# Kernel optimization log

Hardware: AMD Instinct MI355X
Metric: run time of the kernel (lower is better)

## Reference

```python
import jax, jax.numpy as jnp
import numpy as np

HEADS = 16
DIM_HEAD = 64
EPS = 1e-12  # F.normalize default eps


def setup_inputs() -> dict:
    key = jax.random.key(0)
    k1, k2, k3 = jax.random.split(key, 3)
    b, n, dim = 2, 2048, 1024
    dim_inner = HEADS * DIM_HEAD
    x = jax.random.normal(k1, (b, n, dim), dtype=jnp.float32)
    gamma = jnp.ones((dim,), dtype=jnp.float32)
    w_qkv = jax.random.normal(k2, (dim, 3 * dim_inner), dtype=jnp.float32) * 0.02
    w_out = jax.random.normal(k3, (dim_inner, dim), dtype=jnp.float32) * 0.02
    return {"x": x, "gamma": gamma, "w_qkv": w_qkv, "w_out": w_out}


def reference(x, gamma, w_qkv, w_out):
    b, n, dim = x.shape
    h, d = HEADS, DIM_HEAD
    scale = d ** -0.5

    # RMSNorm (lucidrains): F.normalize(x, dim=-1) * dim**0.5 * gamma
    norm = jnp.sqrt(jnp.sum(x * x, axis=-1, keepdims=True))
    xn = x / jnp.maximum(norm, EPS) * (dim ** 0.5) * gamma

    # qkv projection -> [b, n, 3, h, d] -> q/k/v each [b, h, n, d]
    qkv = (xn @ w_qkv).reshape(b, n, 3, h, d)
    qkv = jnp.transpose(qkv, (2, 0, 3, 1, 4))
    q, k, v = qkv[0], qkv[1], qkv[2]

    q = q * scale
    sim = jnp.einsum('bhid,bhjd->bhij', q, k)  # [b, h, n, n]
    causal_mask = jnp.triu(jnp.ones((n, n), dtype=bool), k=1)
    mask_value = -jnp.finfo(sim.dtype).max
    sim = jnp.where(causal_mask, mask_value, sim)
    attn = jax.nn.softmax(sim, axis=-1)
    out = jnp.einsum('bhij,bhjd->bhid', attn, v)  # [b, h, n, d]

    out = jnp.transpose(out, (0, 2, 1, 3)).reshape(b, n, h * d)
    return out @ w_out
```

## Files before the change

kernel.cpp:

```cpp
#include <hip/hip_runtime.h>

typedef __attribute__((ext_vector_type(8))) short bf16x8;
typedef __attribute__((ext_vector_type(4))) short bf16x4;
typedef __attribute__((ext_vector_type(4))) float f32x4;

static __device__ __forceinline__ short f2bf(float f) {
    union { float f; unsigned u; } v; v.f = f;
    unsigned r = v.u + 0x7fffu + ((v.u >> 16) & 1u);
    return (short)(r >> 16);
}

static __device__ __forceinline__ void async_copy16(const short* g, short* l) {
    __builtin_amdgcn_global_load_lds((const __attribute__((address_space(1))) void*)g,
                                     (__attribute__((address_space(3))) void*)l,
                                     16, 0, 0);
}

#define HEADS 16
#define DHEAD 64
#define NSEQ  2048
#define DIM   1024
#define BATCH 2
#define ROWS  (BATCH * NSEQ)
#define NQKV  (3 * HEADS * DHEAD)

__global__ __launch_bounds__(256) void prep_kernel(const float* __restrict__ x,
                                                   const float* __restrict__ gamma,
                                                   const float* __restrict__ w_qkv,
                                                   const float* __restrict__ w_out,
                                                   short* __restrict__ xn,
                                                   short* __restrict__ wqkvT,
                                                   short* __restrict__ woutT) {
    const int blk = blockIdx.x;
    const int t = threadIdx.x;
    __shared__ float tile[64][65];
    __shared__ float part[4];

    if (blk < 1024) {
        const float* in;  short* out;  int C, bx, by;
        if (blk < 768) { in = w_qkv; out = wqkvT; C = NQKV; bx = blk % 48; by = blk / 48; }
        else           { in = w_out; out = woutT; C = DIM;  bx = (blk - 768) & 15; by = (blk - 768) >> 4; }
        const int gx = bx * 64, gy = by * 64;
        const int lc4 = (t & 15) * 4;
        const int lr  = t >> 4;
#pragma unroll
        for (int p = 0; p < 4; ++p) {
            const float4 v = *(const float4*)&in[(size_t)(gy + p * 16 + lr) * C + gx + lc4];
            tile[p * 16 + lr][lc4 + 0] = v.x;
            tile[p * 16 + lr][lc4 + 1] = v.y;
            tile[p * 16 + lr][lc4 + 2] = v.z;
            tile[p * 16 + lr][lc4 + 3] = v.w;
        }
        __syncthreads();
        const int oc  = t >> 2;
        const int or4 = (t & 3) * 16;
#pragma unroll
        for (int j = 0; j < 4; ++j) {
            bf16x4 w;
#pragma unroll
            for (int r = 0; r < 4; ++r) w[r] = f2bf(tile[or4 + j * 4 + r][oc]);
            *(bf16x4*)&out[(size_t)(gx + oc) * DIM + gy + or4 + j * 4] = w;
        }
    } else {
        const int row = blk - 1024;
        const float4 v = ((const float4*)(x + (size_t)row * DIM))[t];
        float s = v.x * v.x + v.y * v.y + v.z * v.z + v.w * v.w;
#pragma unroll
        for (int off = 32; off > 0; off >>= 1) s += __shfl_down(s, off, 64);
        if ((t & 63) == 0) part[t >> 6] = s;
        __syncthreads();
        const float tot = part[0] + part[1] + part[2] + part[3];
        const float scale = 32.0f / fmaxf(sqrtf(tot), 1e-12f);
        const float4 g = ((const float4*)gamma)[t];
        bf16x4 o;
        o[0] = f2bf(v.x * scale * g.x);
        o[1] = f2bf(v.y * scale * g.y);
        o[2] = f2bf(v.z * scale * g.z);
        o[3] = f2bf(v.w * scale * g.w);
        *(bf16x4*)(xn + (size_t)row * DIM + t * 4) = o;
    }
}

template <int MODE, int MT, int NT, int WM, int WN>
__global__ __launch_bounds__(256) void gemm_bt(const short* __restrict__ A,
                                               const short* __restrict__ Bt,
                                               void* __restrict__ Cout,
                                               short* __restrict__ vtOut,
                                               int K, int N) {
    constexpr int TM = WM * MT * 16;
    constexpr int TN = WN * NT * 16;
    __shared__ alignas(16) short lds_a[2][TM * 32];
    __shared__ alignas(16) short lds_b[2][TN * 32];
    const int tid = threadIdx.x;
    const int lane = tid & 63, wid = tid >> 6;
    const int quad = lane >> 4, l16 = lane & 15;
    const int wm = wid / WN, wn = wid % WN;

    const int nx = gridDim.x;
    const int nwg = nx * gridDim.y;
    int flat = blockIdx.y * nx + blockIdx.x;
    if ((nwg & 7) == 0) {
        const int q8 = nwg >> 3;
        flat = (flat & 7) * q8 + (flat >> 3);
    }
    const int mb = (flat / nx) * TM, nb = (flat % nx) * TN;

    f32x4 acc[MT][NT];
#pragma unroll
    for (int i = 0; i < MT; ++i)
#pragma unroll
        for (int j = 0; j < NT; ++j) acc[i][j] = (f32x4){0.f, 0.f, 0.f, 0.f};

    const int lr = lane >> 2;
    const int lc = (lane & 3) * 8;

    auto stage = [&](int kb, int buf) {
#pragma unroll
        for (int c = 0; c < TM / 64; ++c) {
            const int row = c * 64 + wid * 16 + lr;
            async_copy16(&A[(size_t)(mb + row) * K + kb + lc], &lds_a[buf][row * 32 + lc]);
        }
#pragma unroll
        for (int c = 0; c < TN / 64; ++c) {
            const int row = c * 64 + wid * 16 + lr;
            async_copy16(&Bt[(size_t)(nb + row) * K + kb + lc], &lds_b[buf][row * 32 + lc]);
        }
    };

    stage(0, 0);
    __syncthreads();

    int cur = 0;
    for (int kb = 0; kb < K; kb += 32) {
        if (kb + 32 < K) stage(kb + 32, cur ^ 1);

        bf16x8 af[MT], bfr[NT];
#pragma unroll
        for (int mt = 0; mt < MT; ++mt)
            af[mt] = *(const bf16x8*)&lds_a[cur][(wm * MT * 16 + mt * 16 + l16) * 32 + quad * 8];
#pragma unroll
        for (int nt = 0; nt < NT; ++nt)
            bfr[nt] = *(const bf16x8*)&lds_b[cur][(wn * NT * 16 + nt * 16 + l16) * 32 + quad * 8];
#pragma unroll
        for (int mt = 0; mt < MT; ++mt)
#pragma unroll
            for (int nt = 0; nt < NT; ++nt)
                acc[mt][nt] = __builtin_amdgcn_mfma_f32_16x16x32_bf16(af[mt], bfr[nt],
                                                                      acc[mt][nt], 0, 0, 0);

        __syncthreads();
        cur ^= 1;
    }

#pragma unroll
    for (int mt = 0; mt < MT; ++mt) {
#pragma unroll
        for (int nt = 0; nt < NT; ++nt) {
            const int grow0 = mb + wm * MT * 16 + mt * 16 + quad * 4;
            const int gcol  = nb + wn * NT * 16 + nt * 16 + l16;
            if (MODE == 0) {
                const int s3 = gcol >> 10, rem = gcol & 1023;
                const int hh = rem >> 6, dd = rem & 63;
                const int bb = grow0 >> 11, npos0 = grow0 & 2047;
                if (s3 == 2) {
                    bf16x4 vw;
#pragma unroll
                    for (int r = 0; r < 4; ++r) vw[r] = f2bf(acc[mt][nt][r]);
                    *(bf16x4*)&vtOut[((size_t)(bb * 16 + hh) * 64 + dd) * 2048 + npos0] = vw;
                } else {
                    const float sc = (s3 == 0) ? 0.125f : 1.0f;
#pragma unroll
                    for (int r = 0; r < 4; ++r)
                        ((short*)Cout)[(size_t)((s3 * 32 + bb * 16 + hh) * 2048 + npos0 + r) * 64 +
                                       dd] = f2bf(acc[mt][nt][r] * sc);
                }
            } else {
#pragma unroll
                for (int r = 0; r < 4; ++r)
                    ((float*)Cout)[(size_t)(grow0 + r) * N + gcol] = acc[mt][nt][r];
            }
        }
    }
}

__global__ __launch_bounds__(256, 3) void attn_kernel(const short* __restrict__ qg,
                                                      const short* __restrict__ kg,
                                                      const short* __restrict__ vtg,
                                                      short* __restrict__ og) {
    const int tid = threadIdx.x;
    const int wid = tid >> 6, lane = tid & 63;
    const int quad = lane >> 4, l16 = lane & 15;
    const int blk = blockIdx.x;
    const int qt = 15 - (blk >> 5);
    const int bh = blk & 31;
    const size_t base = (size_t)bh * (NSEQ * DHEAD);
    const int bb = bh >> 4, hh = bh & 15;
    const int qbase = qt * 128 + wid * 32;
    const int ntiles = 2 * qt + 2;

    __shared__ alignas(16) short kA[2][2048], kB[2][2048];
    __shared__ alignas(16) short vA[2][2048], vB[2][2048];
    __shared__ alignas(16) short pbuf[4][32 * 72];
    short* const pb = pbuf[wid];

    const int sr = tid >> 2;
    const int sc = (tid & 3) * 8;
    auto stage = [&](int t, short (&KB_)[2][2048], short (&VB_)[2][2048]) {
        const int kb = t * 64;
        async_copy16(&kg[base + (size_t)(kb + sr) * 64 + sc],      &KB_[0][sr * 32 + sc]);
        async_copy16(&kg[base + (size_t)(kb + sr) * 64 + 32 + sc], &KB_[1][sr * 32 + sc]);
        async_copy16(&vtg[base + (size_t)sr * 2048 + kb + sc],      &VB_[0][sr * 32 + sc]);
        async_copy16(&vtg[base + (size_t)sr * 2048 + kb + 32 + sc], &VB_[1][sr * 32 + sc]);
    };

    bf16x8 qf[2][2];
#pragma unroll
    for (int qn = 0; qn < 2; ++qn)
#pragma unroll
        for (int kh = 0; kh < 2; ++kh)
            qf[qn][kh] = *(const bf16x8*)&qg[base + (size_t)(qbase + qn * 16 + l16) * DHEAD +
                                            kh * 32 + quad * 8];

    float li[2] = {0.f, 0.f};
    f32x4 accO[2][4];
#pragma unroll
    for (int qn = 0; qn < 2; ++qn)
#pragma unroll
        for (int nc = 0; nc < 4; ++nc) accO[qn][nc] = (f32x4){0.f, 0.f, 0.f, 0.f};

    auto tile_step = [&](const short (&KB_)[2][2048], const short (&VB_)[2][2048], int t) {
        const int kb = t * 64;
        f32x4 sf[2][4];
#pragma unroll
        for (int m = 0; m < 4; ++m) {
            const bf16x8 kf0 = *(const bf16x8*)&KB_[0][(m * 16 + l16) * 32 + quad * 8];
            const bf16x8 kf1 = *(const bf16x8*)&KB_[1][(m * 16 + l16) * 32 + quad * 8];
#pragma unroll
            for (int qn = 0; qn < 2; ++qn) {
                f32x4 z = (f32x4){0.f, 0.f, 0.f, 0.f};
                z = __builtin_amdgcn_mfma_f32_16x16x32_bf16(kf0, qf[qn][0], z, 0, 0, 0);
                sf[qn][m] = __builtin_amdgcn_mfma_f32_16x16x32_bf16(kf1, qf[qn][1], z, 0, 0, 0);
            }
        }
        if (kb + 64 > qbase) {
#pragma unroll
            for (int qn = 0; qn < 2; ++qn) {
                const int myq = qbase + qn * 16 + l16;
#pragma unroll
                for (int m = 0; m < 4; ++m)
#pragma unroll
                    for (int r = 0; r < 4; ++r)
                        if (kb + m * 16 + quad * 4 + r > myq) sf[qn][m][r] = -3.0e38f;
            }
        }
#pragma unroll
        for (int qn = 0; qn < 2; ++qn) {
            float rs = 0.f;
#pragma unroll
            for (int m = 0; m < 4; ++m) {
                bf16x4 pw;
#pragma unroll
                for (int r = 0; r < 4; ++r) {
                    const float p = __expf(sf[qn][m][r]);
                    rs += p;
                    pw[r] = f2bf(p);
                }
                *(bf16x4*)&pb[(qn * 16 + l16) * 72 + m * 16 + quad * 4] = pw;
            }
            li[qn] += rs;
        }
        bf16x8 pf[2][2];
#pragma unroll
        for (int qn = 0; qn < 2; ++qn)
#pragma unroll
            for (int ks = 0; ks < 2; ++ks)
                pf[qn][ks] = *(const bf16x8*)&pb[(qn * 16 + l16) * 72 + ks * 32 + quad * 8];
#pragma unroll
        for (int nc = 0; nc < 4; ++nc) {
            const bf16x8 vf0 = *(const bf16x8*)&VB_[0][(nc * 16 + l16) * 32 + quad * 8];
            const bf16x8 vf1 = *(const bf16x8*)&VB_[1][(nc * 16 + l16) * 32 + quad * 8];
#pragma unroll
            for (int qn = 0; qn < 2; ++qn) {
                accO[qn][nc] = __builtin_amdgcn_mfma_f32_16x16x32_bf16(vf0, pf[qn][0],
                                                                      accO[qn][nc], 0, 0, 0);
                accO[qn][nc] = __builtin_amdgcn_mfma_f32_16x16x32_bf16(vf1, pf[qn][1],
                                                                      accO[qn][nc], 0, 0, 0);
            }
        }
    };

    stage(0, kA, vA);
    __syncthreads();
    for (int t = 0; t < ntiles; t += 2) {
        stage(t + 1, kB, vB);
        tile_step(kA, vA, t);
        __syncthreads();
        if (t + 2 < ntiles) stage(t + 2, kA, vA);
        tile_step(kB, vB, t + 1);
        __syncthreads();
    }

#pragma unroll
    for (int qn = 0; qn < 2; ++qn) {
        li[qn] += __shfl_xor(li[qn], 16, 64);
        li[qn] += __shfl_xor(li[qn], 32, 64);
        const float inv = 1.0f / li[qn];
        const int npos = qbase + qn * 16 + l16;
#pragma unroll
        for (int nc = 0; nc < 4; ++nc) {
            bf16x4 ow;
#pragma unroll
            for (int r = 0; r < 4; ++r) ow[r] = f2bf(accO[qn][nc][r] * inv);
            *(bf16x4*)&og[(size_t)(bb * 2048 + npos) * 1024 + hh * 64 + nc * 16 + quad * 4] = ow;
        }
    }
}

extern "C" void kernel_launch(void* const* d_in, const int* in_sizes, int n_in,
                              void* d_out, int out_size, void* d_ws, size_t ws_size,
                              hipStream_t stream) {
    const float* x     = (const float*)d_in[0];
    const float* gamma = (const float*)d_in[1];
    const float* w_qkv = (const float*)d_in[2];
    const float* w_out = (const float*)d_in[3];
    float* out = (float*)d_out;
    char* ws = (char*)d_ws;

    short* xn     = (short*)(ws);
    short* wqkvT  = (short*)(ws + 8388608);
    short* woutT  = (short*)(ws + 14680064);
    short* q      = (short*)(ws + 16777216);
    short* k      = q + 32 * 2048 * 64;
    short* vt     = k + 32 * 2048 * 64;
    short* attn   = (short*)(ws + 41943040);

    prep_kernel<<<5120, 256, 0, stream>>>(x, gamma, w_qkv, w_out, xn, wqkvT, woutT);
    gemm_bt<0, 4, 4, 2, 2><<<dim3(NQKV / 128, ROWS / 128), 256, 0, stream>>>(xn, wqkvT, q, vt,
                                                                             DIM, NQKV);
    attn_kernel<<<512, 256, 0, stream>>>(q, k, vt, attn);
    gemm_bt<1, 2, 4, 4, 1><<<dim3(DIM / 64, ROWS / 128), 256, 0, stream>>>(attn, woutT, out,
                                                                           nullptr, DIM, DIM);
}
```

Baseline: 176.2 us.

## Keep softmax probabilities in registers via permlane swaps instead of LDS round-trip

Converts the exp'd attention probabilities to packed bf16 with the hardware v_cvt_pk_bf16_f32 instruction and rearranges them into the MFMA B-operand layout with v_permlane32/16_swap, so the per-wave LDS scratch buffer is no longer needed. This removes LDS writes and reads per tile and frees shared memory, which may raise occupancy. The block-to-query-tile mapping also changes so that blocks beyond 256 walk the tiles in ascending order, pairing heavy and light causal tiles. The risk is that the lane permutation must exactly match the previous LDS layout, or the results will be wrong.

```diff
diff --git a/kernel.cpp b/kernel.cpp
--- a/kernel.cpp
+++ b/kernel.cpp
@@ -191,7 +191,7 @@
     const int wid = tid >> 6, lane = tid & 63;
     const int quad = lane >> 4, l16 = lane & 15;
     const int blk = blockIdx.x;
-    const int qt = 15 - (blk >> 5);
+    const int qt = (blk < 256) ? (15 - (blk >> 5)) : ((blk - 256) >> 5);
     const int bh = blk & 31;
     const size_t base = (size_t)bh * (NSEQ * DHEAD);
     const int bb = bh >> 4, hh = bh & 15;
@@ -200,8 +200,6 @@
 
     __shared__ alignas(16) short kA[2][2048], kB[2][2048];
     __shared__ alignas(16) short vA[2][2048], vB[2][2048];
-    __shared__ alignas(16) short pbuf[4][32 * 72];
-    short* const pb = pbuf[wid];
 
     const int sr = tid >> 2;
     const int sc = (tid & 3) * 8;
@@ -253,19 +251,19 @@
                         if (kb + m * 16 + quad * 4 + r > myq) sf[qn][m][r] = -3.0e38f;
             }
         }
+        unsigned c0[2][4], c1[2][4];
 #pragma unroll
         for (int qn = 0; qn < 2; ++qn) {
             float rs = 0.f;
 #pragma unroll
             for (int m = 0; m < 4; ++m) {
-                bf16x4 pw;
-#pragma unroll
-                for (int r = 0; r < 4; ++r) {
-                    const float p = __expf(sf[qn][m][r]);
-                    rs += p;
-                    pw[r] = f2bf(p);
-                }
-                *(bf16x4*)&pb[(qn * 16 + l16) * 72 + m * 16 + quad * 4] = pw;
+                const float p0 = __expf(sf[qn][m][0]);
+                const float p1 = __expf(sf[qn][m][1]);
+                const float p2 = __expf(sf[qn][m][2]);
+                const float p3 = __expf(sf[qn][m][3]);
+                rs += (p0 + p1) + (p2 + p3);
+                asm("v_cvt_pk_bf16_f32 %0, %1, %2" : "=v"(c0[qn][m]) : "v"(p0), "v"(p1));
+                asm("v_cvt_pk_bf16_f32 %0, %1, %2" : "=v"(c1[qn][m]) : "v"(p2), "v"(p3));
             }
             li[qn] += rs;
         }
@@ -273,8 +271,17 @@
 #pragma unroll
         for (int qn = 0; qn < 2; ++qn)
 #pragma unroll
-            for (int ks = 0; ks < 2; ++ks)
-                pf[qn][ks] = *(const bf16x8*)&pb[(qn * 16 + l16) * 72 + ks * 32 + quad * 8];
+            for (int ks = 0; ks < 2; ++ks) {
+                unsigned a0 = c0[qn][2 * ks], b0 = c0[qn][2 * ks + 1];
+                unsigned a1 = c1[qn][2 * ks], b1 = c1[qn][2 * ks + 1];
+                asm("v_permlane32_swap_b32 %0, %1" : "+v"(a0), "+v"(b0));
+                asm("v_permlane16_swap_b32 %0, %1" : "+v"(a0), "+v"(b0));
+                asm("v_permlane32_swap_b32 %0, %1" : "+v"(a1), "+v"(b1));
+                asm("v_permlane16_swap_b32 %0, %1" : "+v"(a1), "+v"(b1));
+                union { bf16x8 v; unsigned u[4]; } t8;
+                t8.u[0] = a0; t8.u[1] = a1; t8.u[2] = b0; t8.u[3] = b1;
+                pf[qn][ks] = t8.v;
+            }
 #pragma unroll
         for (int nc = 0; nc < 4; ++nc) {
             const bf16x8 vf0 = *(const bf16x8*)&VB_[0][(nc * 16 + l16) * 32 + quad * 8];
```

Result: faster. 165.9 us (-5.9%).
